# Kernel tuning notes

Measured on AMD Instinct MI355X. Metric: run time of the kernel, lower is better.

## Reference

```python
import jax, jax.numpy as jnp
import numpy as np
from jax import lax

D_MODEL = 1024
D_STATE = 16
D_CONV = 4
D_INNER = 2 * D_MODEL
BATCH = 2
SEQ = 1024


def setup_inputs() -> dict:
    key = jax.random.key(0)
    ks = jax.random.split(key, 8)
    std = 0.02
    return {
        "x": jax.random.normal(ks[0], (BATCH, SEQ, D_MODEL), jnp.float32),
        "in_proj_w": jax.random.normal(ks[1], (2 * D_INNER, D_MODEL), jnp.float32) * std,
        "conv_w": jax.random.normal(ks[2], (D_INNER, 1, D_CONV), jnp.float32) * 0.1,
        "x_proj_w": jax.random.normal(ks[3], (D_STATE + 1, D_INNER), jnp.float32) * std,
        "dt_w": jax.random.normal(ks[4], (D_INNER, 1), jnp.float32) * std,
        "dt_b": jnp.zeros((D_INNER,), jnp.float32),
        "A_param": jax.random.normal(ks[5], (D_INNER, D_STATE), jnp.float32) * std,
        "D_param": jnp.ones((D_INNER,), jnp.float32),
        "out_w": jax.random.normal(ks[6], (D_MODEL, D_INNER), jnp.float32) * std,
        "out_b": jnp.zeros((D_MODEL,), jnp.float32),
    }


def _silu(v):
    return v * jax.nn.sigmoid(v)


def _mamba_forward(x, in_proj_w, conv_w, x_proj_w, dt_w, dt_b, A_param, D_param, out_w, out_b):
    B, L, _ = x.shape
    # in_proj: [B,L,2*d_inner]
    xz = jnp.einsum('bld,ed->ble', x, in_proj_w)
    u, z = jnp.split(xz, 2, axis=-1)  # each [B,L,d_inner]
    # depthwise causal conv1d along time
    uc = u.transpose(0, 2, 1)  # [B,d_inner,L]
    uc = lax.conv_general_dilated(
        uc, conv_w, window_strides=(1,), padding=[(D_CONV - 1, D_CONV - 1)],
        dimension_numbers=('NCH', 'OIH', 'NCH'), feature_group_count=D_INNER,
    )[:, :, :L]
    u = _silu(uc.transpose(0, 2, 1))  # [B,L,d_inner]
    # x_proj -> (dt scalar, B coeffs)
    x_dbl = jnp.einsum('bld,ed->ble', u, x_proj_w)  # [B,L,d_state+1]
    dt_in = x_dbl[..., :1]                          # [B,L,1]
    Bmat = x_dbl[..., 1:]                           # [B,L,d_state]
    delta = jax.nn.softplus(dt_in * dt_w[:, 0] + dt_b)  # [B,L,d_inner]
    A = -jnp.exp(A_param)                            # [d_inner,d_state]

    # selective scan (time-major lax.scan)
    def step(h, inp):
        d_t, b_t = inp  # [B,d_inner], [B,d_state]
        h = jnp.exp(A * d_t[..., None]) * h + d_t[..., None] * b_t[:, None, :]
        y = jnp.einsum('bdn,bn->bd', h, b_t)
        return h, y

    h0 = jnp.zeros((B, D_INNER, D_STATE), x.dtype)
    _, ys = lax.scan(step, h0, (delta.transpose(1, 0, 2), Bmat.transpose(1, 0, 2)))
    y = ys.transpose(1, 0, 2) + u * D_param  # [B,L,d_inner]
    y = y * _silu(z)
    return jnp.einsum('bld,ed->ble', y, out_w) + out_b


def reference(x, in_proj_w, conv_w, x_proj_w, dt_w, dt_b, A_param, D_param, out_w, out_b):
    return _mamba_forward(x, in_proj_w, conv_w, x_proj_w, dt_w, dt_b, A_param, D_param, out_w, out_b)
```

## Files before the change

kernel.cpp:

```cpp
#include <hip/hip_runtime.h>
#include <stdint.h>
#include <stddef.h>

#define D_MODEL 1024
#define D_STATE 16
#define D_INNER 2048
#define BATCH   2
#define SEQ     1024
#define MROWS   (BATCH*SEQ)

#define NCH 32
#define TCH (SEQ/NCH)
#define NREC (BATCH*D_INNER*D_STATE)

#define XKS 8
#define XKC (D_INNER/XKS)

#define OM_BF16   0
#define OM_F32    1

typedef __bf16 bf16x8 __attribute__((ext_vector_type(8)));
typedef float  f32x4  __attribute__((ext_vector_type(4)));

__device__ __forceinline__ unsigned short f2bf(float f) {
    unsigned int u = __float_as_uint(f);
    u += 0x7fffu + ((u >> 16) & 1u);
    return (unsigned short)(u >> 16);
}
__device__ __forceinline__ float bf2f(unsigned short v) {
    return __uint_as_float((unsigned int)v << 16);
}

__device__ __forceinline__ void gl_lds16(const unsigned short* g, unsigned short* l) {
    __builtin_amdgcn_global_load_lds(
        (const __attribute__((address_space(1))) unsigned int*)g,
        (__attribute__((address_space(3))) unsigned int*)l, 16, 0, 0);
}

__global__ void cvt_all_kernel(const float* __restrict__ x,
                               const float* __restrict__ w1,
                               const float* __restrict__ w2,
                               const float* __restrict__ xw,
                               unsigned short* __restrict__ xb,
                               unsigned short* __restrict__ wbi,
                               unsigned short* __restrict__ wbo,
                               unsigned short* __restrict__ wbp) {
    int blk = blockIdx.x, tid = threadIdx.x;
    if (blk < 8192) {
        const float* src; unsigned short* dst; int i;
        if (blk < 2048)      { src = x;  dst = xb;  i = blk * 1024 + tid * 4; }
        else if (blk < 6144) { src = w1; dst = wbi; i = (blk - 2048) * 1024 + tid * 4; }
        else                 { src = w2; dst = wbo; i = (blk - 6144) * 1024 + tid * 4; }
        float4 v = *(const float4*)(src + i);
        ushort4 o;
        o.x = f2bf(v.x); o.y = f2bf(v.y); o.z = f2bf(v.z); o.w = f2bf(v.w);
        *(ushort4*)(dst + i) = o;
    } else {
        int id = (blk - 8192) * 256 + tid;
        wbp[id] = (id < 17 * D_INNER) ? f2bf(xw[id]) : (unsigned short)0;
    }
}

template<int NT, bool SPLITK2, int OM, bool SWZ>
__global__ void gemm_bf16_kernel(const unsigned short* __restrict__ A,
                                 const unsigned short* __restrict__ Bw,
                                 void* __restrict__ Cv,
                                 int M, int N, int K) {
    constexpr int NTW = NT / 32;
    constexpr int BCH = NT / 8;
    __shared__ __align__(16) unsigned short Al[2 * 128 * 32];
    __shared__ __align__(16) unsigned short Bl[2 * NT * 32];

    const int tid  = threadIdx.x;
    const int lane = tid & 63;
    const int wid  = tid >> 6;
    const int wm   = wid >> 1;
    const int wn   = wid & 1;
    const int ln   = lane & 15;
    const int q    = lane >> 4;

    int mi, ni;
    if (SWZ) {
        int lin = blockIdx.y * 32 + blockIdx.x;
        int xcd = lin & 7, s = lin >> 3;
        mi = (xcd & 1) * 8 + (s & 7);
        ni = (xcd >> 1) * 8 + (s >> 3);
    } else {
        mi = blockIdx.y; ni = blockIdx.x;
    }
    const int mblk = mi * 128;
    const int nblk = ni * NT;
    const int srow = lane >> 2;
    const int spart = lane & 3;

    const int kbeg = SPLITK2 ? blockIdx.z * (K / 2) : 0;
    const int kend = SPLITK2 ? kbeg + K / 2 : K;

    f32x4 acc[4][NTW] = {};

    for (int k0 = kbeg; k0 < kend; k0 += 64) {
        #pragma unroll
        for (int h = 0; h < 4; ++h) {
            int j = wid * 4 + h;
            int kh = j & 1, rb = j >> 1;
            int row = rb * 16 + srow;
            gl_lds16(A + (size_t)(mblk + row) * K + k0 + kh * 32 + spart * 8,
                     Al + kh * 4096 + rb * 512);
        }
        #pragma unroll
        for (int h = 0; h < BCH / 4; ++h) {
            int j = wid * (BCH / 4) + h;
            int kh = j & 1, rb = j >> 1;
            int row = rb * 16 + srow;
            gl_lds16(Bw + (size_t)(nblk + row) * K + k0 + kh * 32 + spart * 8,
                     Bl + kh * (NT * 32) + rb * 512);
        }
        __syncthreads();

        #pragma unroll
        for (int kh = 0; kh < 2; ++kh) {
            bf16x8 af[4], bfr[NTW];
            #pragma unroll
            for (int mt = 0; mt < 4; ++mt)
                af[mt] = *(const bf16x8*)(Al + kh * 4096 + (wm * 64 + mt * 16 + ln) * 32 + q * 8);
            #pragma unroll
            for (int nt = 0; nt < NTW; ++nt)
                bfr[nt] = *(const bf16x8*)(Bl + kh * (NT * 32) + (wn * (NT/2) + nt * 16 + ln) * 32 + q * 8);
            #pragma unroll
            for (int mt = 0; mt < 4; ++mt)
                #pragma unroll
                for (int nt = 0; nt < NTW; ++nt)
                    acc[mt][nt] = __builtin_amdgcn_mfma_f32_16x16x32_bf16(
                        af[mt], bfr[nt], acc[mt][nt], 0, 0, 0);
        }
        __syncthreads();
    }

    const size_t cofs = SPLITK2 ? (size_t)blockIdx.z * M * N : 0;
    #pragma unroll
    for (int mt = 0; mt < 4; ++mt) {
        #pragma unroll
        for (int nt = 0; nt < NTW; ++nt) {
            int col = nblk + wn * (NT/2) + nt * 16 + ln;
            #pragma unroll
            for (int r = 0; r < 4; ++r) {
                int row = mblk + wm * 64 + mt * 16 + q * 4 + r;
                if (OM == OM_BF16)
                    ((unsigned short*)Cv)[(size_t)row * N + col] = f2bf(acc[mt][nt][r]);
                else
                    ((float*)Cv)[cofs + (size_t)row * N + col] = acc[mt][nt][r];
            }
        }
    }
}

__global__ void splitk_reduce_kernel(const float* __restrict__ part,
                                     const float* __restrict__ bias,
                                     float* __restrict__ out) {
    int i = (blockIdx.x * 256 + threadIdx.x) * 4;
    int n = i & (D_MODEL - 1);
    float4 a = *(const float4*)(part + i);
    float4 b = *(const float4*)(part + (size_t)MROWS * D_MODEL + i);
    float4 bv = *(const float4*)(bias + n);
    float4 o;
    o.x = a.x + b.x + bv.x; o.y = a.y + b.y + bv.y;
    o.z = a.z + b.z + bv.z; o.w = a.w + b.w + bv.w;
    *(float4*)(out + i) = o;
}

__global__ void conv_silu_kernel(const unsigned short* __restrict__ xzb,
                                 const float* __restrict__ conv_w,
                                 unsigned short* __restrict__ ub) {
    int idx = blockIdx.x * blockDim.x + threadIdx.x;
    int d = idx & (D_INNER - 1);
    int m = idx >> 11;
    int l = m & (SEQ - 1);
    const float* w = conv_w + d * 4;
    float s = 0.f;
    #pragma unroll
    for (int j = 0; j < 4; ++j) {
        if (l - j >= 0) s += w[3 - j] * bf2f(xzb[(size_t)(m - j) * 4096 + d]);
    }
    float sig = 1.f / (1.f + __expf(-s));
    ub[idx] = f2bf(s * sig);
}

__global__ void xproj_mfma_kernel(const unsigned short* __restrict__ ub,
                                  const unsigned short* __restrict__ wbp,
                                  float* __restrict__ part) {
    __shared__ __align__(16) unsigned short Al[64 * 64];
    __shared__ __align__(16) unsigned short Bl[32 * 64];

    const int tid  = threadIdx.x;
    const int lane = tid & 63;
    const int wid  = tid >> 6;
    const int ln   = lane & 15;
    const int q    = lane >> 4;
    const int m0   = blockIdx.y * 64;
    const int ks   = blockIdx.x;
    const int srow = lane >> 3;
    const int spart = lane & 7;

    f32x4 acc[2] = {};

    for (int it = 0; it < 4; ++it) {
        int k0 = ks * XKC + it * 64;
        #pragma unroll
        for (int h = 0; h < 2; ++h) {
            int j = wid * 2 + h;
            int row = j * 8 + srow;
            gl_lds16(ub + (size_t)(m0 + row) * D_INNER + k0 + spart * 8, Al + j * 512);
        }
        {
            int row = wid * 8 + srow;
            gl_lds16(wbp + (size_t)row * D_INNER + k0 + spart * 8, Bl + wid * 512);
        }
        __syncthreads();

        bf16x8 af[2], bfr[2][2];
        #pragma unroll
        for (int kh = 0; kh < 2; ++kh) {
            af[kh] = *(const bf16x8*)(Al + (wid * 16 + ln) * 64 + kh * 32 + q * 8);
            bfr[0][kh] = *(const bf16x8*)(Bl + (0 * 16 + ln) * 64 + kh * 32 + q * 8);
            bfr[1][kh] = *(const bf16x8*)(Bl + (1 * 16 + ln) * 64 + kh * 32 + q * 8);
        }
        #pragma unroll
        for (int kh = 0; kh < 2; ++kh) {
            acc[0] = __builtin_amdgcn_mfma_f32_16x16x32_bf16(af[kh], bfr[0][kh], acc[0], 0, 0, 0);
            acc[1] = __builtin_amdgcn_mfma_f32_16x16x32_bf16(af[kh], bfr[1][kh], acc[1], 0, 0, 0);
        }
        __syncthreads();
    }

    #pragma unroll
    for (int nf = 0; nf < 2; ++nf) {
        #pragma unroll
        for (int r = 0; r < 4; ++r) {
            int m = m0 + wid * 16 + q * 4 + r;
            part[((size_t)ks * MROWS + m) * 32 + nf * 16 + ln] = acc[nf][r];
        }
    }
}

__device__ __forceinline__ float softplus_f(float xv) {
    return fmaxf(xv, 0.f) + __logf(1.f + __expf(-fabsf(xv)));
}

__device__ __forceinline__ void reduce_xpt(const float* __restrict__ xpt,
                                           int mg0, int tid,
                                           float* sdt, float* sB) {
    for (int idx = tid; idx < TCH * 17; idx += 256) {
        int t = idx / 17, j = idx % 17;
        float s = 0.f;
        #pragma unroll
        for (int ks = 0; ks < XKS; ++ks)
            s += xpt[((size_t)ks * MROWS + mg0 + t) * 32 + j];
        if (j == 0) sdt[t] = s;
        else        sB[t * D_STATE + (j - 1)] = s;
    }
}

__global__ void scanA_kernel(const float* __restrict__ xpt,
                             const float* __restrict__ dt_w,
                             const float* __restrict__ dt_b,
                             const float* __restrict__ A_param,
                             float* __restrict__ Pg,
                             float* __restrict__ Sg) {
    __shared__ float sdt[TCH];
    __shared__ float sB[TCH * D_STATE];
    const int tid = threadIdx.x;
    const int b = blockIdx.z, c = blockIdx.y;
    const int d = blockIdx.x * 256 + tid;
    const int mg0 = b * SEQ + c * TCH;

    reduce_xpt(xpt, mg0, tid, sdt, sB);
    __syncthreads();

    const float dtw = dt_w[d], dtb = dt_b[d];
    float aA[D_STATE], h[D_STATE];
    #pragma unroll
    for (int n4 = 0; n4 < 4; ++n4) {
        float4 ap = ((const float4*)(A_param + (size_t)d * D_STATE))[n4];
        aA[n4*4+0] = -__expf(ap.x); aA[n4*4+1] = -__expf(ap.y);
        aA[n4*4+2] = -__expf(ap.z); aA[n4*4+3] = -__expf(ap.w);
    }
    #pragma unroll
    for (int n = 0; n < D_STATE; ++n) h[n] = 0.f;
    float tsum = 0.f;

    for (int t = 0; t < TCH; ++t) {
        float sp = softplus_f(sdt[t] * dtw + dtb);
        tsum += sp;
        #pragma unroll
        for (int n = 0; n < D_STATE; ++n) {
            float a = __expf(aA[n] * sp);
            h[n] = a * h[n] + sp * sB[t * D_STATE + n];
        }
    }

    size_t base = (size_t)c * NREC + ((size_t)(b * D_INNER + d)) * D_STATE;
    #pragma unroll
    for (int n4 = 0; n4 < 4; ++n4) {
        float4 pv, sv;
        pv.x = __expf(aA[n4*4+0] * tsum); pv.y = __expf(aA[n4*4+1] * tsum);
        pv.z = __expf(aA[n4*4+2] * tsum); pv.w = __expf(aA[n4*4+3] * tsum);
        sv.x = h[n4*4+0]; sv.y = h[n4*4+1]; sv.z = h[n4*4+2]; sv.w = h[n4*4+3];
        *(float4*)(Pg + base + n4 * 4) = pv;
        *(float4*)(Sg + base + n4 * 4) = sv;
    }
}

__global__ void scanB_kernel(const float* __restrict__ Pg,
                             const float* __restrict__ Sg,
                             float* __restrict__ Hin) {
    int idx = blockIdx.x * 256 + threadIdx.x;
    float h = 0.f;
    #pragma unroll
    for (int c = 0; c < NCH; ++c) {
        size_t o = (size_t)c * NREC + idx;
        Hin[o] = h;
        h = Pg[o] * h + Sg[o];
    }
}

__global__ void scanC_kernel(const float* __restrict__ xpt,
                             const float* __restrict__ dt_w,
                             const float* __restrict__ dt_b,
                             const float* __restrict__ A_param,
                             const float* __restrict__ Hin,
                             const unsigned short* __restrict__ ub,
                             const unsigned short* __restrict__ xzb,
                             const float* __restrict__ Dp,
                             unsigned short* __restrict__ ypb) {
    __shared__ float sdt[TCH];
    __shared__ float sB[TCH * D_STATE];
    const int tid = threadIdx.x;
    const int b = blockIdx.z, c = blockIdx.y;
    const int d = blockIdx.x * 256 + tid;
    const int mg0 = b * SEQ + c * TCH;

    reduce_xpt(xpt, mg0, tid, sdt, sB);
    __syncthreads();

    const float dtw = dt_w[d], dtb = dt_b[d];
    const float Dv = Dp[d];
    float aA[D_STATE], h[D_STATE];
    #pragma unroll
    for (int n4 = 0; n4 < 4; ++n4) {
        float4 ap = ((const float4*)(A_param + (size_t)d * D_STATE))[n4];
        aA[n4*4+0] = -__expf(ap.x); aA[n4*4+1] = -__expf(ap.y);
        aA[n4*4+2] = -__expf(ap.z); aA[n4*4+3] = -__expf(ap.w);
    }
    size_t hbase = (size_t)c * NREC + ((size_t)(b * D_INNER + d)) * D_STATE;
    #pragma unroll
    for (int n4 = 0; n4 < 4; ++n4) {
        float4 hv = *(const float4*)(Hin + hbase + n4 * 4);
        h[n4*4+0] = hv.x; h[n4*4+1] = hv.y; h[n4*4+2] = hv.z; h[n4*4+3] = hv.w;
    }

    for (int t = 0; t < TCH; ++t) {
        float sp = softplus_f(sdt[t] * dtw + dtb);
        float y0 = 0.f, y1 = 0.f, y2 = 0.f, y3 = 0.f;
        #pragma unroll
        for (int n4 = 0; n4 < 4; ++n4) {
            #pragma unroll
            for (int j = 0; j < 4; ++j) {
                int n = n4 * 4 + j;
                float Bv = sB[t * D_STATE + n];
                float a = __expf(aA[n] * sp);
                h[n] = a * h[n] + sp * Bv;
                float p = h[n] * Bv;
                if (n4 == 0) y0 += p; else if (n4 == 1) y1 += p;
                else if (n4 == 2) y2 += p; else y3 += p;
            }
        }
        float y = (y0 + y1) + (y2 + y3);
        size_t m = (size_t)mg0 + t;
        float z  = bf2f(xzb[m * 4096 + D_INNER + d]);
        float sz = z / (1.f + __expf(-z));
        float uv = bf2f(ub[m * D_INNER + d]);
        ypb[m * D_INNER + d] = f2bf((y + uv * Dv) * sz);
    }
}

extern "C" void kernel_launch(void* const* d_in, const int* in_sizes, int n_in,
                              void* d_out, int out_size, void* d_ws, size_t ws_size,
                              hipStream_t stream) {
    const float* x         = (const float*)d_in[0];
    const float* in_proj_w = (const float*)d_in[1];
    const float* conv_w    = (const float*)d_in[2];
    const float* x_proj_w  = (const float*)d_in[3];
    const float* dt_w      = (const float*)d_in[4];
    const float* dt_b      = (const float*)d_in[5];
    const float* A_param   = (const float*)d_in[6];
    const float* D_param   = (const float*)d_in[7];
    const float* out_w     = (const float*)d_in[8];
    const float* out_b     = (const float*)d_in[9];
    float* out = (float*)d_out;

    char* ws = (char*)d_ws;
    unsigned short* xb  = (unsigned short*)(ws);
    unsigned short* wbi = (unsigned short*)(ws + (4u  << 20));
    unsigned short* wbo = (unsigned short*)(ws + (12u << 20));
    unsigned short* xzb = (unsigned short*)(ws + (16u << 20));
    unsigned short* ub  = (unsigned short*)(ws + (32u << 20));
    unsigned short* wbp = (unsigned short*)(ws + (40u << 20));
    float*          xpt = (float*)(ws + (40u << 20) + (512u << 10));
    float*          Pg  = (float*)(ws + (44u << 20));
    float*          Sg  = (float*)(ws + (52u << 20));
    float*          Hin = (float*)(ws + (60u << 20));
    unsigned short* ypb = (unsigned short*)(ws + (68u << 20));
    float*          g2p = (float*)(ws + (76u << 20));

    cvt_all_kernel<<<dim3(8448), 256, 0, stream>>>(
        x, in_proj_w, out_w, x_proj_w, xb, wbi, wbo, wbp);

    gemm_bf16_kernel<128, false, OM_BF16, true><<<dim3(32, 16), 256, 0, stream>>>(
        xb, wbi, xzb, MROWS, 2 * D_INNER, D_MODEL);

    conv_silu_kernel<<<dim3(MROWS * D_INNER / 256), 256, 0, stream>>>(xzb, conv_w, ub);

    xproj_mfma_kernel<<<dim3(XKS, MROWS / 64), 256, 0, stream>>>(ub, wbp, xpt);

    scanA_kernel<<<dim3(D_INNER / 256, NCH, BATCH), 256, 0, stream>>>(
        xpt, dt_w, dt_b, A_param, Pg, Sg);
    scanB_kernel<<<dim3(NREC / 256), 256, 0, stream>>>(Pg, Sg, Hin);
    scanC_kernel<<<dim3(D_INNER / 256, NCH, BATCH), 256, 0, stream>>>(
        xpt, dt_w, dt_b, A_param, Hin, ub, xzb, D_param, ypb);

    gemm_bf16_kernel<64, true, OM_F32, false><<<dim3(1024 / 64, MROWS / 128, 2), 256, 0, stream>>>(
        ypb, wbo, g2p, MROWS, D_MODEL, D_INNER);

    splitk_reduce_kernel<<<dim3(MROWS * D_MODEL / 1024), 256, 0, stream>>>(g2p, out_b, out);
}
```

Measured before the change: 225.4 us.

## Fuse three-phase chunked scan into one cooperative kernel with grid syncs

Replaces the scanA/scanB/scanC kernel sequence with a single cooperative kernel that uses grid-wide barriers between the chunk-summary, cross-chunk carry, and output phases. The xpt reduction to shared memory and the A/dt setup are done once instead of twice. Launch gaps between the phases go away. It also removes the XCD-aware block swizzle from the first GEMM. The fused kernel needs all 512 blocks co-resident and pays for two grid syncs.

```diff
diff --git a/kernel.cpp b/kernel.cpp
--- a/kernel.cpp
+++ b/kernel.cpp
@@ -1,6 +1,9 @@
 #include <hip/hip_runtime.h>
+#include <hip/hip_cooperative_groups.h>
 #include <stdint.h>
 #include <stddef.h>
+
+namespace cg = cooperative_groups;
 
 #define D_MODEL 1024
 #define D_STATE 16
@@ -61,7 +64,7 @@
     }
 }
 
-template<int NT, bool SPLITK2, int OM, bool SWZ>
+template<int NT, bool SPLITK2, int OM>
 __global__ void gemm_bf16_kernel(const unsigned short* __restrict__ A,
                                  const unsigned short* __restrict__ Bw,
                                  void* __restrict__ Cv,
@@ -78,18 +81,8 @@
     const int wn   = wid & 1;
     const int ln   = lane & 15;
     const int q    = lane >> 4;
-
-    int mi, ni;
-    if (SWZ) {
-        int lin = blockIdx.y * 32 + blockIdx.x;
-        int xcd = lin & 7, s = lin >> 3;
-        mi = (xcd & 1) * 8 + (s & 7);
-        ni = (xcd >> 1) * 8 + (s >> 3);
-    } else {
-        mi = blockIdx.y; ni = blockIdx.x;
-    }
-    const int mblk = mi * 128;
-    const int nblk = ni * NT;
+    const int mblk = blockIdx.y * 128;
+    const int nblk = blockIdx.x * NT;
     const int srow = lane >> 2;
     const int spart = lane & 3;
 
@@ -246,26 +239,17 @@
     return fmaxf(xv, 0.f) + __logf(1.f + __expf(-fabsf(xv)));
 }
 
-__device__ __forceinline__ void reduce_xpt(const float* __restrict__ xpt,
-                                           int mg0, int tid,
-                                           float* sdt, float* sB) {
-    for (int idx = tid; idx < TCH * 17; idx += 256) {
-        int t = idx / 17, j = idx % 17;
-        float s = 0.f;
-        #pragma unroll
-        for (int ks = 0; ks < XKS; ++ks)
-            s += xpt[((size_t)ks * MROWS + mg0 + t) * 32 + j];
-        if (j == 0) sdt[t] = s;
-        else        sB[t * D_STATE + (j - 1)] = s;
-    }
-}
-
-__global__ void scanA_kernel(const float* __restrict__ xpt,
-                             const float* __restrict__ dt_w,
-                             const float* __restrict__ dt_b,
-                             const float* __restrict__ A_param,
-                             float* __restrict__ Pg,
-                             float* __restrict__ Sg) {
+__global__ void scan_fused_kernel(const float* __restrict__ xpt,
+                                  const float* __restrict__ dt_w,
+                                  const float* __restrict__ dt_b,
+                                  const float* __restrict__ A_param,
+                                  const unsigned short* __restrict__ ub,
+                                  const unsigned short* __restrict__ xzb,
+                                  const float* __restrict__ Dp,
+                                  float* __restrict__ Pg,
+                                  float* __restrict__ Sg,
+                                  float* __restrict__ Hin,
+                                  unsigned short* __restrict__ ypb) {
     __shared__ float sdt[TCH];
     __shared__ float sB[TCH * D_STATE];
     const int tid = threadIdx.x;
@@ -273,10 +257,19 @@
     const int d = blockIdx.x * 256 + tid;
     const int mg0 = b * SEQ + c * TCH;
 
-    reduce_xpt(xpt, mg0, tid, sdt, sB);
+    for (int idx = tid; idx < TCH * 17; idx += 256) {
+        int t = idx / 17, j = idx % 17;
+        float s = 0.f;
+        #pragma unroll
+        for (int ks = 0; ks < XKS; ++ks)
+            s += xpt[((size_t)ks * MROWS + mg0 + t) * 32 + j];
+        if (j == 0) sdt[t] = s;
+        else        sB[t * D_STATE + (j - 1)] = s;
+    }
     __syncthreads();
 
     const float dtw = dt_w[d], dtb = dt_b[d];
+    const float Dv = Dp[d];
     float aA[D_STATE], h[D_STATE];
     #pragma unroll
     for (int n4 = 0; n4 < 4; ++n4) {
@@ -284,10 +277,10 @@
         aA[n4*4+0] = -__expf(ap.x); aA[n4*4+1] = -__expf(ap.y);
         aA[n4*4+2] = -__expf(ap.z); aA[n4*4+3] = -__expf(ap.w);
     }
+
     #pragma unroll
     for (int n = 0; n < D_STATE; ++n) h[n] = 0.f;
     float tsum = 0.f;
-
     for (int t = 0; t < TCH; ++t) {
         float sp = softplus_f(sdt[t] * dtw + dtb);
         tsum += sp;
@@ -297,7 +290,6 @@
             h[n] = a * h[n] + sp * sB[t * D_STATE + n];
         }
     }
-
     size_t base = (size_t)c * NREC + ((size_t)(b * D_INNER + d)) * D_STATE;
     #pragma unroll
     for (int n4 = 0; n4 < 4; ++n4) {
@@ -308,56 +300,30 @@
         *(float4*)(Pg + base + n4 * 4) = pv;
         *(float4*)(Sg + base + n4 * 4) = sv;
     }
-}
-
-__global__ void scanB_kernel(const float* __restrict__ Pg,
-                             const float* __restrict__ Sg,
-                             float* __restrict__ Hin) {
-    int idx = blockIdx.x * 256 + threadIdx.x;
-    float h = 0.f;
-    #pragma unroll
-    for (int c = 0; c < NCH; ++c) {
-        size_t o = (size_t)c * NREC + idx;
-        Hin[o] = h;
-        h = Pg[o] * h + Sg[o];
-    }
-}
-
-__global__ void scanC_kernel(const float* __restrict__ xpt,
-                             const float* __restrict__ dt_w,
-                             const float* __restrict__ dt_b,
-                             const float* __restrict__ A_param,
-                             const float* __restrict__ Hin,
-                             const unsigned short* __restrict__ ub,
-                             const unsigned short* __restrict__ xzb,
-                             const float* __restrict__ Dp,
-                             unsigned short* __restrict__ ypb) {
-    __shared__ float sdt[TCH];
-    __shared__ float sB[TCH * D_STATE];
-    const int tid = threadIdx.x;
-    const int b = blockIdx.z, c = blockIdx.y;
-    const int d = blockIdx.x * 256 + tid;
-    const int mg0 = b * SEQ + c * TCH;
-
-    reduce_xpt(xpt, mg0, tid, sdt, sB);
-    __syncthreads();
-
-    const float dtw = dt_w[d], dtb = dt_b[d];
-    const float Dv = Dp[d];
-    float aA[D_STATE], h[D_STATE];
+
+    cg::this_grid().sync();
+
+    {
+        int fb = (blockIdx.z * gridDim.y + blockIdx.y) * gridDim.x + blockIdx.x;
+        int gid = fb * 256 + tid;
+        if (gid < NREC) {
+            float hh = 0.f;
+            #pragma unroll
+            for (int cc = 0; cc < NCH; ++cc) {
+                size_t o = (size_t)cc * NREC + gid;
+                Hin[o] = hh;
+                hh = Pg[o] * hh + Sg[o];
+            }
+        }
+    }
+
+    cg::this_grid().sync();
+
     #pragma unroll
     for (int n4 = 0; n4 < 4; ++n4) {
-        float4 ap = ((const float4*)(A_param + (size_t)d * D_STATE))[n4];
-        aA[n4*4+0] = -__expf(ap.x); aA[n4*4+1] = -__expf(ap.y);
-        aA[n4*4+2] = -__expf(ap.z); aA[n4*4+3] = -__expf(ap.w);
-    }
-    size_t hbase = (size_t)c * NREC + ((size_t)(b * D_INNER + d)) * D_STATE;
-    #pragma unroll
-    for (int n4 = 0; n4 < 4; ++n4) {
-        float4 hv = *(const float4*)(Hin + hbase + n4 * 4);
+        float4 hv = *(const float4*)(Hin + base + n4 * 4);
         h[n4*4+0] = hv.x; h[n4*4+1] = hv.y; h[n4*4+2] = hv.z; h[n4*4+3] = hv.w;
     }
-
     for (int t = 0; t < TCH; ++t) {
         float sp = softplus_f(sdt[t] * dtw + dtb);
         float y0 = 0.f, y1 = 0.f, y2 = 0.f, y3 = 0.f;
@@ -415,20 +381,23 @@
     cvt_all_kernel<<<dim3(8448), 256, 0, stream>>>(
         x, in_proj_w, out_w, x_proj_w, xb, wbi, wbo, wbp);
 
-    gemm_bf16_kernel<128, false, OM_BF16, true><<<dim3(32, 16), 256, 0, stream>>>(
+    gemm_bf16_kernel<128, false, OM_BF16><<<dim3(32, 16), 256, 0, stream>>>(
         xb, wbi, xzb, MROWS, 2 * D_INNER, D_MODEL);
 
     conv_silu_kernel<<<dim3(MROWS * D_INNER / 256), 256, 0, stream>>>(xzb, conv_w, ub);
 
     xproj_mfma_kernel<<<dim3(XKS, MROWS / 64), 256, 0, stream>>>(ub, wbp, xpt);
 
-    scanA_kernel<<<dim3(D_INNER / 256, NCH, BATCH), 256, 0, stream>>>(
-        xpt, dt_w, dt_b, A_param, Pg, Sg);
-    scanB_kernel<<<dim3(NREC / 256), 256, 0, stream>>>(Pg, Sg, Hin);
-    scanC_kernel<<<dim3(D_INNER / 256, NCH, BATCH), 256, 0, stream>>>(
-        xpt, dt_w, dt_b, A_param, Hin, ub, xzb, D_param, ypb);
-
-    gemm_bf16_kernel<64, true, OM_F32, false><<<dim3(1024 / 64, MROWS / 128, 2), 256, 0, stream>>>(
+    {
+        void* args[] = { (void*)&xpt, (void*)&dt_w, (void*)&dt_b, (void*)&A_param,
+                         (void*)&ub, (void*)&xzb, (void*)&D_param,
+                         (void*)&Pg, (void*)&Sg, (void*)&Hin, (void*)&ypb };
+        hipLaunchCooperativeKernel((const void*)scan_fused_kernel,
+                                   dim3(D_INNER / 256, NCH, BATCH), dim3(256),
+                                   args, 0, stream);
+    }
+
+    gemm_bf16_kernel<64, true, OM_F32><<<dim3(1024 / 64, MROWS / 128, 2), 256, 0, stream>>>(
         ypb, wbo, g2p, MROWS, D_MODEL, D_INNER);
 
     splitk_reduce_kernel<<<dim3(MROWS * D_MODEL / 1024), 256, 0, stream>>>(g2p, out_b, out);
```

Measured after the change: 343.7 us. 52.5% more time.
